# Optimization experiments

Hardware: AMD Instinct MI355X
Metric: run time of the kernel (lower is better)

## Reference

```python
import jax, jax.numpy as jnp
import numpy as np

ROPE_BASE = 10000.0

def _rope_tables(seq_len, head_dim, dtype):
    inv_freq = 1.0 / (ROPE_BASE ** (jnp.arange(0, head_dim, 2, dtype=jnp.float32) / head_dim))
    t = jnp.arange(seq_len, dtype=jnp.float32)
    freqs = jnp.einsum('s,d->sd', t, inv_freq)  # [S, D/2]
    return jnp.cos(freqs).astype(dtype), jnp.sin(freqs).astype(dtype)

def _apply_rope(x, cos, sin):
    # x: [B, H, S, D]; cos/sin: [S, D/2]
    half = x.shape[-1] // 2
    x1, x2 = x[..., :half], x[..., half:]
    c = cos[None, None, :, :]
    s = sin[None, None, :, :]
    return jnp.concatenate([x1 * c - x2 * s, x1 * s + x2 * c], axis=-1)

def setup_inputs() -> dict:
    key = jax.random.key(0)
    k1, k2, k3 = jax.random.split(key, 3)
    B, S, dim = 4, 2048, 1024
    x = jax.random.normal(k1, (B, S, dim), dtype=jnp.float32)
    Wqkv = jax.random.normal(k2, (3 * dim, dim), dtype=jnp.float32) * (1.0 / np.sqrt(dim))
    Wout = jax.random.normal(k3, (dim, dim), dtype=jnp.float32) * (1.0 / np.sqrt(dim))
    mask = jnp.tril(jnp.ones((S, S), dtype=bool))[None, None, :, :]  # causal [1,1,S,S]
    return {"x": x, "mask": mask, "Wqkv": Wqkv, "Wout": Wout, "n_heads": 16}

def reference(x, mask, Wqkv, Wout, n_heads):
    B, S, dim = x.shape
    H = n_heads
    D = dim // H
    qkv = jnp.einsum('bsd,ed->bse', x, Wqkv)             # [B,S,3*dim]
    qkv = qkv.reshape(B, S, 3, H, D)
    q = jnp.transpose(qkv[:, :, 0], (0, 2, 1, 3))        # [B,H,S,D]
    k = jnp.transpose(qkv[:, :, 1], (0, 2, 1, 3))
    v = jnp.transpose(qkv[:, :, 2], (0, 2, 1, 3))
    cos, sin = _rope_tables(S, D, x.dtype)
    q = _apply_rope(q, cos, sin)
    k = _apply_rope(k, cos, sin)
    scale = 1.0 / np.sqrt(D).astype(np.float32)
    scores = jnp.einsum('bhsd,bhtd->bhst', q, k) * scale  # [B,H,S,S]
    scores = jnp.where(mask, scores, -jnp.inf)
    attn = jax.nn.softmax(scores, axis=-1)
    out = jnp.einsum('bhst,bhtd->bhsd', attn, v)          # [B,H,S,D]
    out = jnp.transpose(out, (0, 2, 1, 3)).reshape(B, S, dim)
    return jnp.einsum('bsd,ed->bse', out, Wout)
```

## Files before the change

kernel.cpp:

```cpp
#include <hip/hip_runtime.h>
#include <math.h>


typedef __attribute__((ext_vector_type(8))) __bf16 bf16x8;
typedef __attribute__((ext_vector_type(8))) short  short8;
typedef __attribute__((ext_vector_type(4))) short  s16x4;
typedef __attribute__((ext_vector_type(4))) float  f32x4;

#define MFMA16(a, b, c) __builtin_amdgcn_mfma_f32_16x16x32_bf16((a), (b), (c), 0, 0, 0)

static constexpr int    BATCH = 4;
static constexpr int    SEQ   = 2048;
static constexpr int    DIM   = 1024;
static constexpr int    NH    = 16;
static constexpr int    HD    = 64;
static constexpr size_t BHSD  = (size_t)BATCH * NH * SEQ * HD;
static constexpr float  NEGINF = -1e9f;
static constexpr int    PS_LD  = 72;

__device__ __forceinline__ short f2bf(float f) {
    union { float f; unsigned u; } v; v.f = f;
    unsigned r = v.u + 0x7fffu + ((v.u >> 16) & 1u);
    return (short)(r >> 16);
}

__device__ __forceinline__ short8 cvt8(const f32x4 lo, const f32x4 hi) {
    short8 r;
    r[0] = f2bf(lo[0]); r[1] = f2bf(lo[1]); r[2] = f2bf(lo[2]); r[3] = f2bf(lo[3]);
    r[4] = f2bf(hi[0]); r[5] = f2bf(hi[1]); r[6] = f2bf(hi[2]); r[7] = f2bf(hi[3]);
    return r;
}

template <bool F32>
__device__ __forceinline__ short8 ld8(const void* p, size_t row, int K, int k) {
    if constexpr (F32) {
        const float* f = (const float*)p;
        f32x4 lo = *(const f32x4*)&f[row * (size_t)K + k];
        f32x4 hi = *(const f32x4*)&f[row * (size_t)K + k + 4];
        return cvt8(lo, hi);
    } else {
        const short* s = (const short*)p;
        return *(const short8*)&s[row * (size_t)K + k];
    }
}

__device__ __forceinline__ void gload16(const void* g, void* lds) {
    __builtin_amdgcn_global_load_lds(
        (const __attribute__((address_space(1))) void*)g,
        (__attribute__((address_space(3))) void*)lds, 16, 0, 0);
}

__global__ __launch_bounds__(256) void prep_kernel(
    const float* __restrict__ X, const float* __restrict__ Wq,
    const float* __restrict__ Wo, short* __restrict__ Xb,
    short* __restrict__ Wqb, short* __restrict__ Wob,
    float* __restrict__ cosT, float* __restrict__ sinT) {
    const int stride = gridDim.x * blockDim.x;
    for (int idx = blockIdx.x * blockDim.x + threadIdx.x; idx < 3211264; idx += stride) {
        if (idx < 3145728) {
            const float* src; short* dst; int off;
            if (idx < 2097152)      { src = X;  dst = Xb;  off = idx; }
            else if (idx < 2883584) { src = Wq; dst = Wqb; off = idx - 2097152; }
            else                    { src = Wo; dst = Wob; off = idx - 2883584; }
            f32x4 v = *(const f32x4*)&src[(size_t)off * 4];
            s16x4 r;
            r[0] = f2bf(v[0]); r[1] = f2bf(v[1]); r[2] = f2bf(v[2]); r[3] = f2bf(v[3]);
            *(s16x4*)&dst[(size_t)off * 4] = r;
        } else {
            int r = idx - 3145728;
            int s = r >> 5, d = r & 31;
            float ang = (float)s * __expf(-0.28782313662425574f * (float)d);
            float sn, cs;
            sincosf(ang, &sn, &cs);
            cosT[r] = cs; sinT[r] = sn;
        }
    }
}

template <bool AF32, bool BF32>
__device__ __forceinline__ void gemm128_core(
    const void* __restrict__ A, const void* __restrict__ B, int K,
    short* As, short* Bs, int bm, int bn, f32x4 acc[4][4]) {
    const int tid  = threadIdx.x;
    const int lane = tid & 63;
    const int wave = tid >> 6;
    const int quad = lane >> 4;
    const int col  = lane & 15;
    const int wm   = (wave & 1) * 64;
    const int wn   = (wave >> 1) * 64;

    const int r0 = tid >> 2;
    const int r1 = (tid + 256) >> 2;
    const int ko = (tid & 3) * 8;

#pragma unroll
    for (int i = 0; i < 4; ++i)
#pragma unroll
        for (int j = 0; j < 4; ++j) acc[i][j] = f32x4{0.f, 0.f, 0.f, 0.f};

#pragma unroll 1
    for (int k0 = 0; k0 < K; k0 += 32) {
        short8 a0 = ld8<AF32>(A, (size_t)(bm + r0), K, k0 + ko);
        short8 a1 = ld8<AF32>(A, (size_t)(bm + r1), K, k0 + ko);
        short8 b0 = ld8<BF32>(B, (size_t)(bn + r0), K, k0 + ko);
        short8 b1 = ld8<BF32>(B, (size_t)(bn + r1), K, k0 + ko);
        __syncthreads();
        *(short8*)&As[tid * 8]         = a0;
        *(short8*)&As[(tid + 256) * 8] = a1;
        *(short8*)&Bs[tid * 8]         = b0;
        *(short8*)&Bs[(tid + 256) * 8] = b1;
        __syncthreads();

        bf16x8 af[4], bfr[4];
#pragma unroll
        for (int i = 0; i < 4; ++i)
            af[i] = *(const bf16x8*)&As[(wm + i * 16 + col) * 32 + quad * 8];
#pragma unroll
        for (int j = 0; j < 4; ++j)
            bfr[j] = *(const bf16x8*)&Bs[(wn + j * 16 + col) * 32 + quad * 8];
#pragma unroll
        for (int i = 0; i < 4; ++i)
#pragma unroll
            for (int j = 0; j < 4; ++j)
                acc[i][j] = MFMA16(af[i], bfr[j], acc[i][j]);
    }
}

__device__ __forceinline__ void gemm128_lds(
    const short* __restrict__ A, const short* __restrict__ B, int K,
    short* As, short* Bs, int bm, int bn, f32x4 acc[4][4]) {
    const int tid  = threadIdx.x;
    const int lane = tid & 63;
    const int wave = tid >> 6;
    const int quad = lane >> 4;
    const int col  = lane & 15;
    const int wm   = (wave & 1) * 64;
    const int wn   = (wave >> 1) * 64;

    const int r0 = tid >> 2;
    const int r1 = r0 + 64;
    const int ko = (tid & 3) * 8;

    const short* A0 = &A[(size_t)(bm + r0) * K + ko];
    const short* A1 = &A[(size_t)(bm + r1) * K + ko];
    const short* B0 = &B[(size_t)(bn + r0) * K + ko];
    const short* B1 = &B[(size_t)(bn + r1) * K + ko];

    short* As0 = &As[wave * 512];
    short* As1 = &As[2048 + wave * 512];
    short* Bs0 = &Bs[wave * 512];
    short* Bs1 = &Bs[2048 + wave * 512];

#pragma unroll
    for (int i = 0; i < 4; ++i)
#pragma unroll
        for (int j = 0; j < 4; ++j) acc[i][j] = f32x4{0.f, 0.f, 0.f, 0.f};

#pragma unroll 1
    for (int k0 = 0; k0 < K; k0 += 32) {
        __syncthreads();
        gload16(A0 + k0, As0);
        gload16(A1 + k0, As1);
        gload16(B0 + k0, Bs0);
        gload16(B1 + k0, Bs1);
        __syncthreads();

        bf16x8 af[4], bfr[4];
#pragma unroll
        for (int i = 0; i < 4; ++i)
            af[i] = *(const bf16x8*)&As[(wm + i * 16 + col) * 32 + quad * 8];
#pragma unroll
        for (int j = 0; j < 4; ++j)
            bfr[j] = *(const bf16x8*)&Bs[(wn + j * 16 + col) * 32 + quad * 8];
#pragma unroll
        for (int i = 0; i < 4; ++i)
#pragma unroll
            for (int j = 0; j < 4; ++j)
                acc[i][j] = MFMA16(af[i], bfr[j], acc[i][j]);
    }
}

template <bool PRE>
__global__ __launch_bounds__(256, 2) void qkv_rope_kernel(
    const void* __restrict__ X, const void* __restrict__ W,
    const float* __restrict__ cosT, const float* __restrict__ sinT,
    short* __restrict__ Qo, short* __restrict__ Ko, short* __restrict__ VT) {
    __shared__ __align__(16) short As[128 * 32];
    __shared__ __align__(16) short Bs[128 * 32];
    const int bm = blockIdx.y * 128, bn = blockIdx.x * 128;
    const int lane = threadIdx.x & 63, wave = threadIdx.x >> 6;
    const int quad = lane >> 4, col = lane & 15;
    const int wm = (wave & 1) * 64, wn = (wave >> 1) * 64;

    f32x4 acc[4][4];
    if constexpr (PRE)
        gemm128_lds((const short*)X, (const short*)W, 1024, As, Bs, bm, bn, acc);
    else
        gemm128_core<true, true>(X, W, 1024, As, Bs, bm, bn, acc);

    const int n0    = bn + wn;
    const int which = n0 >> 10;
    const int h     = (n0 >> 6) & 15;

    if (which == 2) {
#pragma unroll
        for (int i = 0; i < 4; ++i) {
            int    m = bm + wm + i * 16 + quad * 4;
            int    b = m >> 11, s = m & 2047;
            size_t rowb = (size_t)(b * NH + h) * HD;
#pragma unroll
            for (int j = 0; j < 4; ++j) {
                int   d = j * 16 + col;
                s16x4 pk;
                pk[0] = f2bf(acc[i][j][0]); pk[1] = f2bf(acc[i][j][1]);
                pk[2] = f2bf(acc[i][j][2]); pk[3] = f2bf(acc[i][j][3]);
                *(s16x4*)&VT[(rowb + d) * SEQ + s] = pk;
            }
        }
    } else {
        short* dst = which ? Ko : Qo;
#pragma unroll
        for (int i = 0; i < 4; ++i)
#pragma unroll
            for (int reg = 0; reg < 4; ++reg) {
                int    m = bm + wm + i * 16 + quad * 4 + reg;
                int    b = m >> 11, s = m & 2047;
                size_t base = ((size_t)(b * NH + h) * SEQ + s) * HD;
#pragma unroll
                for (int j = 0; j < 2; ++j) {
                    int   d1 = j * 16 + col;
                    float sn, cs;
                    if constexpr (PRE) {
                        cs = cosT[(s << 5) + d1];
                        sn = sinT[(s << 5) + d1];
                    } else {
                        float inv = __expf(-0.28782313662425574f * (float)d1);
                        sincosf((float)s * inv, &sn, &cs);
                    }
                    float x1 = acc[i][j][reg];
                    float x2 = acc[i][j + 2][reg];
                    dst[base + d1]      = f2bf(x1 * cs - x2 * sn);
                    dst[base + d1 + 32] = f2bf(x1 * sn + x2 * cs);
                }
            }
    }
}

__global__ __launch_bounds__(256, 2) void attn_kernel(
    const short* __restrict__ Q, const short* __restrict__ K,
    const short* __restrict__ VT, short* __restrict__ att) {
    const int b = blockIdx.z, h = blockIdx.y;
    const int tid = threadIdx.x, wave = tid >> 6, lane = tid & 63;
    const int quad = lane >> 4, col = lane & 15;
    const size_t hoff = (size_t)(b * NH + h) * SEQ * HD;
    const short* Qp  = Q + hoff;
    const short* Kp  = K + hoff;
    const short* VTp = VT + hoff;

    __shared__ __align__(16) short Kt[64 * 64];
    __shared__ __align__(16) short Vt[64 * 64];
    __shared__ __align__(16) short Ps[4 * 16 * PS_LD];

    const int r0 = tid >> 3;
    const int r1 = r0 + 32;
    const int c8 = (tid & 7) * 8;
    const int cs = c8 ^ ((r0 & 7) << 3);
    const int swc = (col & 7) << 3;
    const int cA  = (quad * 8) ^ swc;
    const int cB  = (32 + quad * 8) ^ swc;
    short* Pw = &Ps[wave * 16 * PS_LD];

#pragma unroll 1
    for (int pass = 0; pass < 2; ++pass) {
        const int qt = pass ? 31 - (int)blockIdx.x : (int)blockIdx.x;
        const int q0 = qt * 64 + wave * 16;

        bf16x8 aq0 = *(const bf16x8*)&Qp[(q0 + col) * HD + quad * 8];
        bf16x8 aq1 = *(const bf16x8*)&Qp[(q0 + col) * HD + 32 + quad * 8];

        float m_i[4], l_i[4];
        f32x4 o[4];
#pragma unroll
        for (int r = 0; r < 4; ++r) { m_i[r] = NEGINF; l_i[r] = 0.f; o[r] = f32x4{0.f, 0.f, 0.f, 0.f}; }

        short8 ka = *(const short8*)&Kp[r0 * HD + c8];
        short8 kb = *(const short8*)&Kp[r1 * HD + c8];
        short8 va = *(const short8*)&VTp[(size_t)r0 * SEQ + c8];
        short8 vb = *(const short8*)&VTp[(size_t)r1 * SEQ + c8];

#pragma unroll 1
        for (int t = 0; t <= qt; ++t) {
            const int kt = t * 64;
            __syncthreads();
            *(short8*)&Kt[r0 * 64 + cs] = ka;
            *(short8*)&Kt[r1 * 64 + cs] = kb;
            *(short8*)&Vt[r0 * 64 + cs] = va;
            *(short8*)&Vt[r1 * 64 + cs] = vb;
            __syncthreads();

            if (t < qt) {
                const int kn = kt + 64;
                ka = *(const short8*)&Kp[(kn + r0) * HD + c8];
                kb = *(const short8*)&Kp[(kn + r1) * HD + c8];
                va = *(const short8*)&VTp[(size_t)r0 * SEQ + kn + c8];
                vb = *(const short8*)&VTp[(size_t)r1 * SEQ + kn + c8];
            }

            float p[4][4];
#pragma unroll
            for (int jn = 0; jn < 4; ++jn) {
                f32x4  s  = f32x4{0.f, 0.f, 0.f, 0.f};
                bf16x8 b0 = *(const bf16x8*)&Kt[(jn * 16 + col) * 64 + cA];
                bf16x8 b1 = *(const bf16x8*)&Kt[(jn * 16 + col) * 64 + cB];
                s = MFMA16(aq0, b0, s);
                s = MFMA16(aq1, b1, s);
                if (t == qt) {
#pragma unroll
                    for (int reg = 0; reg < 4; ++reg) {
                        int qr = wave * 16 + quad * 4 + reg;
                        int kc = jn * 16 + col;
                        p[jn][reg] = (kc <= qr) ? s[reg] * 0.125f : NEGINF;
                    }
                } else {
#pragma unroll
                    for (int reg = 0; reg < 4; ++reg) p[jn][reg] = s[reg] * 0.125f;
                }
            }

            float alpha[4];
#pragma unroll
            for (int reg = 0; reg < 4; ++reg) {
                float mx = fmaxf(fmaxf(p[0][reg], p[1][reg]), fmaxf(p[2][reg], p[3][reg]));
#pragma unroll
                for (int off = 8; off >= 1; off >>= 1) mx = fmaxf(mx, __shfl_xor(mx, off, 64));
                float mn   = fmaxf(m_i[reg], mx);
                alpha[reg] = __expf(m_i[reg] - mn);
                float rs = 0.f;
#pragma unroll
                for (int jn = 0; jn < 4; ++jn) { p[jn][reg] = __expf(p[jn][reg] - mn); rs += p[jn][reg]; }
#pragma unroll
                for (int off = 8; off >= 1; off >>= 1) rs += __shfl_xor(rs, off, 64);
                l_i[reg] = l_i[reg] * alpha[reg] + rs;
                m_i[reg] = mn;
            }
#pragma unroll
            for (int jd = 0; jd < 4; ++jd)
#pragma unroll
                for (int reg = 0; reg < 4; ++reg) o[jd][reg] *= alpha[reg];

#pragma unroll
            for (int jn = 0; jn < 4; ++jn)
#pragma unroll
                for (int reg = 0; reg < 4; ++reg)
                    Pw[(quad * 4 + reg) * PS_LD + jn * 16 + col] = f2bf(p[jn][reg]);

            bf16x8 ap0 = *(const bf16x8*)&Pw[col * PS_LD + quad * 8];
            bf16x8 ap1 = *(const bf16x8*)&Pw[col * PS_LD + 32 + quad * 8];
#pragma unroll
            for (int jd = 0; jd < 4; ++jd) {
                bf16x8 bv0 = *(const bf16x8*)&Vt[(jd * 16 + col) * 64 + cA];
                bf16x8 bv1 = *(const bf16x8*)&Vt[(jd * 16 + col) * 64 + cB];
                o[jd] = MFMA16(ap0, bv0, o[jd]);
                o[jd] = MFMA16(ap1, bv1, o[jd]);
            }
        }

#pragma unroll
        for (int jd = 0; jd < 4; ++jd)
#pragma unroll
            for (int reg = 0; reg < 4; ++reg) {
                int s = q0 + quad * 4 + reg;
                att[((size_t)(b * SEQ + s)) * DIM + h * HD + jd * 16 + col] =
                    f2bf(o[jd][reg] / l_i[reg]);
            }
    }
}

template <bool PRE>
__global__ __launch_bounds__(256, 2) void out_gemm_kernel(
    const short* __restrict__ A, const void* __restrict__ W,
    float* __restrict__ out) {
    __shared__ __align__(16) short As[128 * 32];
    __shared__ __align__(16) short Bs[128 * 32];
    const int bm = blockIdx.y * 128, bn = blockIdx.x * 128;
    const int lane = threadIdx.x & 63, wave = threadIdx.x >> 6;
    const int quad = lane >> 4, col = lane & 15;
    const int wm = (wave & 1) * 64, wn = (wave >> 1) * 64;

    f32x4 acc[4][4];
    if constexpr (PRE)
        gemm128_lds(A, (const short*)W, 1024, As, Bs, bm, bn, acc);
    else
        gemm128_core<false, true>(A, W, 1024, As, Bs, bm, bn, acc);

#pragma unroll
    for (int i = 0; i < 4; ++i)
#pragma unroll
        for (int reg = 0; reg < 4; ++reg) {
            int    m    = bm + wm + i * 16 + quad * 4 + reg;
            size_t base = (size_t)m * DIM + bn + wn;
#pragma unroll
            for (int j = 0; j < 4; ++j)
                out[base + j * 16 + col] = acc[i][j][reg];
        }
}

extern "C" void kernel_launch(void* const* d_in, const int* in_sizes, int n_in,
                              void* d_out, int out_size, void* d_ws, size_t ws_size,
                              hipStream_t stream) {
    const float* x    = nullptr;
    const float* Wqkv = nullptr;
    const float* Wout = nullptr;
    for (int i = 0; i < n_in; ++i) {
        switch (in_sizes[i]) {
            case 8388608: x    = (const float*)d_in[i]; break;
            case 3145728: Wqkv = (const float*)d_in[i]; break;
            case 1048576: Wout = (const float*)d_in[i]; break;
            default: break;
        }
    }
    if (!x || !Wqkv || !Wout) return;

    short* Q  = (short*)d_ws;
    short* K  = Q + BHSD;
    short* VT = K + BHSD;
    float* out = (float*)d_out;

    const size_t need_pre = (size_t)4 * BHSD * sizeof(short)
                          + BHSD * sizeof(short)
                          + (size_t)3145728 * sizeof(short)
                          + (size_t)1048576 * sizeof(short)
                          + (size_t)2 * 65536 * sizeof(float);

    if (ws_size >= need_pre) {
        short* att  = VT + BHSD;
        short* Xb   = att + BHSD;
        short* Wqb  = Xb + BHSD;
        short* Wob  = Wqb + 3145728;
        float* cosT = (float*)(Wob + 1048576);
        float* sinT = cosT + 65536;

        prep_kernel<<<dim3(2048), 256, 0, stream>>>(x, Wqkv, Wout, Xb, Wqb, Wob, cosT, sinT);
        qkv_rope_kernel<true><<<dim3(24, 64), 256, 0, stream>>>(Xb, Wqb, cosT, sinT, Q, K, VT);
        attn_kernel<<<dim3(16, NH, BATCH), 256, 0, stream>>>(Q, K, VT, att);
        out_gemm_kernel<true><<<dim3(8, 64), 256, 0, stream>>>(att, Wob, out);
    } else {
        qkv_rope_kernel<false><<<dim3(24, 64), 256, 0, stream>>>(
            x, Wqkv, nullptr, nullptr, Q, K, VT);

        const bool direct = ws_size >= (size_t)4 * BHSD * sizeof(short);
        short* att_dst = direct ? (VT + BHSD) : (short*)d_out;
        attn_kernel<<<dim3(16, NH, BATCH), 256, 0, stream>>>(Q, K, VT, att_dst);

        short* att = att_dst;
        if (!direct) {
            att = (short*)d_ws;
            hipMemcpyAsync(att, att_dst, BHSD * sizeof(short), hipMemcpyDeviceToDevice, stream);
        }
        out_gemm_kernel<false><<<dim3(8, 64), 256, 0, stream>>>(att, Wout, out);
    }
}
```

Measured before the change: 308.7 us.

## Stage QKV epilogue through LDS for coalesced stores and swizzle attention block order

The QKV+RoPE epilogue now writes each wave's bf16 results into a per-wave LDS tile, then issues 16-byte vector stores to Q, K and V-transposed. This replaces the previous scattered 2-byte and 8-byte global stores. Separately, the attention launch becomes a 1D grid whose block index is remapped so that consecutive blocks spread across heads and batches, aiming for better L2 locality and balance across XCDs. The cost is extra LDS (20KB per block), which could reduce occupancy of the GEMM kernel.

```diff
diff --git a/kernel.cpp b/kernel.cpp
--- a/kernel.cpp
+++ b/kernel.cpp
@@ -17,6 +17,7 @@
 static constexpr size_t BHSD  = (size_t)BATCH * NH * SEQ * HD;
 static constexpr float  NEGINF = -1e9f;
 static constexpr int    PS_LD  = 72;
+static constexpr int    EP_W   = 2560;
 
 __device__ __forceinline__ short f2bf(float f) {
     union { float f; unsigned u; } v; v.f = f;
@@ -187,6 +188,7 @@
     short* __restrict__ Qo, short* __restrict__ Ko, short* __restrict__ VT) {
     __shared__ __align__(16) short As[128 * 32];
     __shared__ __align__(16) short Bs[128 * 32];
+    __shared__ __align__(16) short Ep[4 * EP_W];
     const int bm = blockIdx.y * 128, bn = blockIdx.x * 128;
     const int lane = threadIdx.x & 63, wave = threadIdx.x >> 6;
     const int quad = lane >> 4, col = lane & 15;
@@ -201,55 +203,79 @@
     const int n0    = bn + wn;
     const int which = n0 >> 10;
     const int h     = (n0 >> 6) & 15;
+    short* Lw = &Ep[wave * EP_W];
 
     if (which == 2) {
 #pragma unroll
-        for (int i = 0; i < 4; ++i) {
-            int    m = bm + wm + i * 16 + quad * 4;
-            int    b = m >> 11, s = m & 2047;
-            size_t rowb = (size_t)(b * NH + h) * HD;
-#pragma unroll
-            for (int j = 0; j < 4; ++j) {
-                int   d = j * 16 + col;
-                s16x4 pk;
-                pk[0] = f2bf(acc[i][j][0]); pk[1] = f2bf(acc[i][j][1]);
-                pk[2] = f2bf(acc[i][j][2]); pk[3] = f2bf(acc[i][j][3]);
-                *(s16x4*)&VT[(rowb + d) * SEQ + s] = pk;
-            }
+        for (int ih = 0; ih < 2; ++ih) {
+            const int m0 = bm + wm + ih * 32;
+            const int b0 = m0 >> 11, s0 = m0 & 2047;
+#pragma unroll
+            for (int ii = 0; ii < 2; ++ii) {
+                const int i  = ih * 2 + ii;
+                const int sl = ii * 16 + quad * 4;
+#pragma unroll
+                for (int j = 0; j < 4; ++j) {
+                    s16x4 pk;
+                    pk[0] = f2bf(acc[i][j][0]); pk[1] = f2bf(acc[i][j][1]);
+                    pk[2] = f2bf(acc[i][j][2]); pk[3] = f2bf(acc[i][j][3]);
+                    *(s16x4*)&Lw[(j * 16 + col) * 40 + sl] = pk;
+                }
+            }
+            const size_t rowb = (size_t)(b0 * NH + h) * HD;
+            short* dv = &VT[(rowb + lane) * (size_t)SEQ + s0];
+#pragma unroll
+            for (int k = 0; k < 4; ++k)
+                *(short8*)&dv[k * 8] = *(const short8*)&Lw[lane * 40 + k * 8];
         }
     } else {
         short* dst = which ? Ko : Qo;
 #pragma unroll
-        for (int i = 0; i < 4; ++i)
-#pragma unroll
-            for (int reg = 0; reg < 4; ++reg) {
-                int    m = bm + wm + i * 16 + quad * 4 + reg;
-                int    b = m >> 11, s = m & 2047;
-                size_t base = ((size_t)(b * NH + h) * SEQ + s) * HD;
-#pragma unroll
-                for (int j = 0; j < 2; ++j) {
-                    int   d1 = j * 16 + col;
-                    float sn, cs;
-                    if constexpr (PRE) {
-                        cs = cosT[(s << 5) + d1];
-                        sn = sinT[(s << 5) + d1];
-                    } else {
-                        float inv = __expf(-0.28782313662425574f * (float)d1);
-                        sincosf((float)s * inv, &sn, &cs);
+        for (int ih = 0; ih < 2; ++ih) {
+            const int m0 = bm + wm + ih * 32;
+            const int b0 = m0 >> 11, s0 = m0 & 2047;
+#pragma unroll
+            for (int ii = 0; ii < 2; ++ii) {
+                const int i = ih * 2 + ii;
+#pragma unroll
+                for (int reg = 0; reg < 4; ++reg) {
+                    const int r = ii * 16 + quad * 4 + reg;
+                    const int s = s0 + r;
+#pragma unroll
+                    for (int j = 0; j < 2; ++j) {
+                        const int d1 = j * 16 + col;
+                        float sn, cs;
+                        if constexpr (PRE) {
+                            cs = cosT[(s << 5) + d1];
+                            sn = sinT[(s << 5) + d1];
+                        } else {
+                            float inv = __expf(-0.28782313662425574f * (float)d1);
+                            sincosf((float)s * inv, &sn, &cs);
+                        }
+                        float x1 = acc[i][j][reg];
+                        float x2 = acc[i][j + 2][reg];
+                        Lw[r * 72 + d1]      = f2bf(x1 * cs - x2 * sn);
+                        Lw[r * 72 + d1 + 32] = f2bf(x1 * sn + x2 * cs);
                     }
-                    float x1 = acc[i][j][reg];
-                    float x2 = acc[i][j + 2][reg];
-                    dst[base + d1]      = f2bf(x1 * cs - x2 * sn);
-                    dst[base + d1 + 32] = f2bf(x1 * sn + x2 * cs);
                 }
             }
+            const int rr = lane >> 1, c0 = (lane & 1) * 32;
+            short* dq = dst + ((size_t)(b0 * NH + h) * SEQ + s0) * HD + rr * HD + c0;
+#pragma unroll
+            for (int k = 0; k < 4; ++k)
+                *(short8*)&dq[k * 8] = *(const short8*)&Lw[rr * 72 + c0 + k * 8];
+        }
     }
 }
 
 __global__ __launch_bounds__(256, 2) void attn_kernel(
     const short* __restrict__ Q, const short* __restrict__ K,
     const short* __restrict__ VT, short* __restrict__ att) {
-    const int b = blockIdx.z, h = blockIdx.y;
+    const int id = (int)blockIdx.x;
+    const int sw = (id & 7) * 128 + (id >> 3);
+    const int bx = sw & 15;
+    const int h  = (sw >> 4) & 15;
+    const int b  = sw >> 8;
     const int tid = threadIdx.x, wave = tid >> 6, lane = tid & 63;
     const int quad = lane >> 4, col = lane & 15;
     const size_t hoff = (size_t)(b * NH + h) * SEQ * HD;
@@ -272,7 +298,7 @@
 
 #pragma unroll 1
     for (int pass = 0; pass < 2; ++pass) {
-        const int qt = pass ? 31 - (int)blockIdx.x : (int)blockIdx.x;
+        const int qt = pass ? 31 - bx : bx;
         const int q0 = qt * 64 + wave * 16;
 
         bf16x8 aq0 = *(const bf16x8*)&Qp[(q0 + col) * HD + quad * 8];
@@ -442,7 +468,7 @@
 
         prep_kernel<<<dim3(2048), 256, 0, stream>>>(x, Wqkv, Wout, Xb, Wqb, Wob, cosT, sinT);
         qkv_rope_kernel<true><<<dim3(24, 64), 256, 0, stream>>>(Xb, Wqb, cosT, sinT, Q, K, VT);
-        attn_kernel<<<dim3(16, NH, BATCH), 256, 0, stream>>>(Q, K, VT, att);
+        attn_kernel<<<dim3(1024), 256, 0, stream>>>(Q, K, VT, att);
         out_gemm_kernel<true><<<dim3(8, 64), 256, 0, stream>>>(att, Wob, out);
     } else {
         qkv_rope_kernel<false><<<dim3(24, 64), 256, 0, stream>>>(
@@ -450,7 +476,7 @@
 
         const bool direct = ws_size >= (size_t)4 * BHSD * sizeof(short);
         short* att_dst = direct ? (VT + BHSD) : (short*)d_out;
-        attn_kernel<<<dim3(16, NH, BATCH), 256, 0, stream>>>(Q, K, VT, att_dst);
+        attn_kernel<<<dim3(1024), 256, 0, stream>>>(Q, K, VT, att_dst);
 
         short* att = att_dst;
         if (!direct) {
```

After: 332.1 us. +7.6%, slower.
